# Kernel optimization log

Hardware: AMD Instinct MI355X
Metric: run time of the kernel (lower is better)

## Reference

```python
import jax, jax.numpy as jnp
import numpy as np

N_AG, N_ANCH, C_FEAT, D_ANCH, N_HEAD = 6, 1024, 256, 8, 8


def _ln(x, g, b, eps=1e-5):
    m = x.mean(-1, keepdims=True)
    v = jnp.mean((x - m) ** 2, axis=-1, keepdims=True)
    return (x - m) / jnp.sqrt(v + eps) * g + b


def _forward(i2j_anchor, b_anchor, b_feature, transform_matrix, lidar_range, anchor_embed,
             cls_w1, cls_b1, cls_g1, cls_bb1, cls_w2, cls_b2, cls_g2, cls_bb2, cls_w3, cls_b3,
             bn_g, bn_b, te_w1, te_b1, te_w2, te_b2, ae_w, ae_b, ae_g, ae_bb,
             wq, bq, wk, bk, wv, bv, wo, bo, norm_g, norm_b, K, step):
    N, A, D = b_anchor.shape
    C = b_feature.shape[-1]
    H = N_HEAD
    dh = C // H
    # refinement.cls_layers: [Linear,ReLU,LN] x2 + Linear->1, then sigmoid
    x = _ln(jax.nn.relu(b_feature @ cls_w1 + cls_b1), cls_g1, cls_bb1)
    x = _ln(jax.nn.relu(x @ cls_w2 + cls_b2), cls_g2, cls_bb2)
    roi = jax.nn.sigmoid(x @ cls_w3 + cls_b3)[..., 0]                       # [N,A]
    top_scores, top_idx = jax.lax.top_k(roi, K)                             # [N,K]
    conf_mask = top_scores > 0.7
    neigh_feat = jnp.take_along_axis(b_feature, top_idx[:, :, None], axis=1)  # [N,K,C]
    idx4 = jnp.broadcast_to(top_idx[None, :, :, None], (N, N, K, D))
    i2j = jnp.take_along_axis(i2j_anchor, idx4, axis=2)                     # [N,N,K,D]
    # diagonal removal (static off-diagonal index pattern)
    off = np.nonzero(~np.eye(N, dtype=bool))
    i2j_rm = i2j[off].reshape(N, (N - 1) * K, D)
    tm_rm = transform_matrix[off].reshape(N, N - 1, 4, 4)
    nf_rm = jnp.broadcast_to(neigh_feat[None], (N, N, K, C))[off].reshape(N, (N - 1) * K, C)
    cm_rm = jnp.broadcast_to(conf_mask[None, :, :, None], (N, N, K, 1))[off].reshape(N, (N - 1) * K, 1)
    # transform encoding: BatchNorm1d(12) (training batch stats) + Mlp(12->256->256)
    flat = tm_rm[..., :3, :].reshape(-1, 12)                                # rows 0..2 flattened = stacked 12 entries
    mu = flat.mean(0)
    var = jnp.mean((flat - mu) ** 2, axis=0)
    bn = (flat - mu) / jnp.sqrt(var + 1e-5) * bn_g + bn_b
    te = jax.nn.relu(bn @ te_w1 + te_b1) @ te_w2 + te_b2                    # [N*(N-1),C]
    te = jnp.repeat(te.reshape(N, N - 1, 1, C), K, axis=2).reshape(N, (N - 1) * K, C)
    ae = _ln(jax.nn.relu(i2j_rm @ ae_w + ae_b), ae_g, ae_bb)
    key_pos = ae + te  # computed in the original forward but unused downstream
    # oriented bbox -> axis-aligned corners
    s = jnp.abs(b_anchor[..., 6])
    c = jnp.abs(b_anchor[..., 7])
    dims = jnp.exp(b_anchor[..., 3:6])
    half = jnp.stack([0.5 * (dims[..., 0] * c + dims[..., 1] * s),
                      0.5 * (dims[..., 0] * s + dims[..., 1] * c),
                      0.5 * dims[..., 2]], axis=-1)
    minp = b_anchor[..., :3] - half                                         # [N,A,3]
    maxp = b_anchor[..., :3] + half
    # ego <- neighbor cross attention (residual, query_pos added to query)
    ego = jnp.broadcast_to(b_feature[0:1], (N - 1, A, C))
    neigh = b_feature[1:]
    qpos = jnp.broadcast_to(anchor_embed[0:1], (N - 1, A, C))
    q = ((ego + qpos) @ wq + bq).reshape(N - 1, A, H, dh)
    k = (neigh @ wk + bk).reshape(N - 1, A, H, dh)
    v = (neigh @ wv + bv).reshape(N - 1, A, H, dh)
    scores = jnp.einsum('bqhd,bkhd->bhqk', q, k) / jnp.sqrt(jnp.asarray(dh, q.dtype))
    attn = jax.nn.softmax(scores, axis=-1)
    o = jnp.einsum('bhqk,bkhd->bqhd', attn, v).reshape(N - 1, A, C) @ wo + bo
    res = jnp.sum(ego + o, axis=0, keepdims=True)                           # [1,A,C]
    _ = _ln(res, norm_g, norm_b)  # self.norm(res): computed then overwritten in original
    # confidence-masked neighbor features, bbox-containment aggregation
    nf_rm = nf_rm * cm_rm.astype(nf_rm.dtype)
    pts = i2j_rm[..., :3]                                                   # [N,M,3], M=(N-1)*K
    inside = jnp.all((pts[:, None] >= minp[:, :, None]) & (pts[:, None] <= maxp[:, :, None]), axis=-1)  # [N,A,M]
    cnt = inside.sum(-1)
    agg = jnp.einsum('nam,nmc->nac', inside.astype(nf_rm.dtype), nf_rm) / jnp.maximum(cnt, 1).astype(nf_rm.dtype)[..., None]
    out_feat = res + agg                                                    # [1,A,C] + [N,A,C] -> [N,A,C]
    return b_anchor, out_feat


def setup_inputs():
    N, A, C, D = N_AG, N_ANCH, C_FEAT, D_ANCH
    ks = jax.random.split(jax.random.key(0), 16)
    def nrm(i, shp, s=1.0):
        return s * jax.random.normal(ks[i], shp, dtype=jnp.float32)
    z = lambda *shp: jnp.zeros(shp, jnp.float32)
    o = lambda *shp: jnp.ones(shp, jnp.float32)
    return {
        'i2j_anchor': nrm(0, (N, N, A, D)), 'b_anchor': nrm(1, (N, A, D)),
        'b_feature': nrm(2, (N, A, C)), 'transform_matrix': nrm(3, (N, N, 4, 4)),
        'lidar_range': z(6), 'anchor_embed': nrm(4, (N, A, C)),
        'cls_w1': nrm(5, (C, C), 0.05), 'cls_b1': z(C), 'cls_g1': o(C), 'cls_bb1': z(C),
        'cls_w2': nrm(6, (C, C), 0.05), 'cls_b2': z(C), 'cls_g2': o(C), 'cls_bb2': z(C),
        'cls_w3': nrm(7, (C, 1), 0.05), 'cls_b3': z(1),
        'bn_g': o(12), 'bn_b': z(12),
        'te_w1': nrm(8, (12, C), 0.05), 'te_b1': z(C), 'te_w2': nrm(9, (C, C), 0.05), 'te_b2': z(C),
        'ae_w': nrm(10, (D, C), 0.05), 'ae_b': z(C), 'ae_g': o(C), 'ae_bb': z(C),
        'wq': nrm(11, (C, C), 0.05), 'bq': z(C), 'wk': nrm(12, (C, C), 0.05), 'bk': z(C),
        'wv': nrm(13, (C, C), 0.05), 'bv': z(C), 'wo': nrm(14, (C, C), 0.05), 'bo': z(C),
        'norm_g': o(C), 'norm_b': z(C),
        'K': 256, 'step': 1,
    }


def reference(i2j_anchor, b_anchor, b_feature, transform_matrix, lidar_range, anchor_embed,
              cls_w1, cls_b1, cls_g1, cls_bb1, cls_w2, cls_b2, cls_g2, cls_bb2, cls_w3, cls_b3,
              bn_g, bn_b, te_w1, te_b1, te_w2, te_b2, ae_w, ae_b, ae_g, ae_bb,
              wq, bq, wk, bk, wv, bv, wo, bo, norm_g, norm_b, K, step):
    return _forward(i2j_anchor, b_anchor, b_feature, transform_matrix, lidar_range, anchor_embed,
                    cls_w1, cls_b1, cls_g1, cls_bb1, cls_w2, cls_b2, cls_g2, cls_bb2, cls_w3, cls_b3,
                    bn_g, bn_b, te_w1, te_b1, te_w2, te_b2, ae_w, ae_b, ae_g, ae_bb,
                    wq, bq, wk, bk, wv, bv, wo, bo, norm_g, norm_b, K, step)
```

## Files before the change

kernel.cpp:

```cpp
#include <hip/hip_runtime.h>


#define N_AG   6
#define N_ANCH 1024
#define C_FEAT 256
#define D_ANCH 8
#define KTOP   256
#define NM     1280
#define NR     40960
#define ZROW   393216
#define AC     262144

__device__ __forceinline__ float waveSum(float v) {
  #pragma unroll
  for (int off = 32; off; off >>= 1) v += __shfl_down(v, off);
  return v;
}

__global__ __launch_bounds__(256) void cls_kernel(
    const float* __restrict__ bf,
    const float* __restrict__ w1, const float* __restrict__ b1,
    const float* __restrict__ g1, const float* __restrict__ bb1,
    const float* __restrict__ w2, const float* __restrict__ b2,
    const float* __restrict__ g2, const float* __restrict__ bb2,
    const float* __restrict__ w3, const float* __restrict__ b3,
    float* __restrict__ roi)
{
  __shared__ float xin[8][256];
  __shared__ float xout[8][256];
  __shared__ float stats[8][2];
  const int t = threadIdx.x;
  const int wid = t >> 6, lane = t & 63;
  const int r0 = blockIdx.x * 8;

  for (int r = 0; r < 8; ++r) xin[r][t] = bf[(r0 + r) * 256 + t];

  const float G1 = g1[t], B1 = bb1[t], G2 = g2[t], B2 = bb2[t];
  float acc[8];

  #pragma unroll
  for (int r = 0; r < 8; ++r) acc[r] = b1[t];
  __syncthreads();
  for (int kk = 0; kk < 256; kk += 4) {
    const float wa = w1[(kk+0)*256+t], wb = w1[(kk+1)*256+t];
    const float wc = w1[(kk+2)*256+t], wd = w1[(kk+3)*256+t];
    #pragma unroll
    for (int r = 0; r < 8; ++r) {
      const float4 xv = *(const float4*)&xin[r][kk];
      acc[r] = fmaf(xv.x, wa, fmaf(xv.y, wb, fmaf(xv.z, wc, fmaf(xv.w, wd, acc[r]))));
    }
  }
  #pragma unroll
  for (int r = 0; r < 8; ++r) xout[r][t] = fmaxf(acc[r], 0.f);
  __syncthreads();
  for (int r = wid; r < 8; r += 4) {
    float s = xout[r][lane] + xout[r][lane+64] + xout[r][lane+128] + xout[r][lane+192];
    s = waveSum(s);
    if (lane == 0) stats[r][0] = s * (1.f/256.f);
  }
  __syncthreads();
  for (int r = wid; r < 8; r += 4) {
    const float m = stats[r][0];
    const float d0 = xout[r][lane]-m, d1 = xout[r][lane+64]-m;
    const float d2 = xout[r][lane+128]-m, d3 = xout[r][lane+192]-m;
    const float s = waveSum(d0*d0 + d1*d1 + d2*d2 + d3*d3);
    if (lane == 0) stats[r][1] = 1.f / sqrtf(s * (1.f/256.f) + 1e-5f);
  }
  __syncthreads();
  #pragma unroll
  for (int r = 0; r < 8; ++r)
    xin[r][t] = (xout[r][t] - stats[r][0]) * stats[r][1] * G1 + B1;
  __syncthreads();

  #pragma unroll
  for (int r = 0; r < 8; ++r) acc[r] = b2[t];
  for (int kk = 0; kk < 256; kk += 4) {
    const float wa = w2[(kk+0)*256+t], wb = w2[(kk+1)*256+t];
    const float wc = w2[(kk+2)*256+t], wd = w2[(kk+3)*256+t];
    #pragma unroll
    for (int r = 0; r < 8; ++r) {
      const float4 xv = *(const float4*)&xin[r][kk];
      acc[r] = fmaf(xv.x, wa, fmaf(xv.y, wb, fmaf(xv.z, wc, fmaf(xv.w, wd, acc[r]))));
    }
  }
  __syncthreads();
  #pragma unroll
  for (int r = 0; r < 8; ++r) xout[r][t] = fmaxf(acc[r], 0.f);
  __syncthreads();
  for (int r = wid; r < 8; r += 4) {
    float s = xout[r][lane] + xout[r][lane+64] + xout[r][lane+128] + xout[r][lane+192];
    s = waveSum(s);
    if (lane == 0) stats[r][0] = s * (1.f/256.f);
  }
  __syncthreads();
  for (int r = wid; r < 8; r += 4) {
    const float m = stats[r][0];
    const float d0 = xout[r][lane]-m, d1 = xout[r][lane+64]-m;
    const float d2 = xout[r][lane+128]-m, d3 = xout[r][lane+192]-m;
    const float s = waveSum(d0*d0 + d1*d1 + d2*d2 + d3*d3);
    if (lane == 0) stats[r][1] = 1.f / sqrtf(s * (1.f/256.f) + 1e-5f);
  }
  __syncthreads();
  const float w3t = w3[t], b30 = b3[0];
  #pragma unroll
  for (int r = 0; r < 8; ++r) {
    const float xn = (xout[r][t] - stats[r][0]) * stats[r][1] * G2 + B2;
    xin[r][t] = xn * w3t;
  }
  __syncthreads();
  for (int r = wid; r < 8; r += 4) {
    float s = xin[r][lane] + xin[r][lane+64] + xin[r][lane+128] + xin[r][lane+192];
    s = waveSum(s);
    if (lane == 0) roi[r0 + r] = 1.f / (1.f + expf(-(s + b30)));
  }
}

__global__ __launch_bounds__(512) void topk_kernel(
    const float* __restrict__ roi, int* __restrict__ top_idx, float* __restrict__ conf)
{
  __shared__ unsigned long long keys[1024];
  const int t = threadIdx.x;
  const int ag = blockIdx.x;
  for (int i = t; i < 1024; i += 512) {
    const unsigned int bits = __float_as_uint(roi[ag * 1024 + i]);
    keys[i] = ((unsigned long long)bits << 10) | (unsigned long long)(1023 - i);
  }
  __syncthreads();
  for (int k = 2; k <= 1024; k <<= 1) {
    for (int j = k >> 1; j > 0; j >>= 1) {
      const int i = ((t & ~(j - 1)) << 1) | (t & (j - 1));
      const int p = i | j;
      const unsigned long long a = keys[i], b = keys[p];
      const bool up = ((i & k) == 0);
      if ((a < b) == up) { keys[i] = b; keys[p] = a; }
      __syncthreads();
    }
  }
  if (t < 256) {
    const unsigned long long key = keys[t];
    const int idx = 1023 - (int)(key & 1023ull);
    const float sc = __uint_as_float((unsigned int)(key >> 10));
    top_idx[ag * 256 + t] = idx;
    conf[ag * 256 + t] = (sc > 0.7f) ? 1.0f : 0.0f;
  }
}

__global__ __launch_bounds__(256) void gather_prep_kernel(
    const float* __restrict__ bf, const int* __restrict__ top_idx,
    const float* __restrict__ conf, const float* __restrict__ ba,
    const float* __restrict__ i2j,
    float* __restrict__ mfeat, float* __restrict__ out,
    float* __restrict__ minmax, float* __restrict__ pts)
{
  const int t = threadIdx.x;
  const int blk = blockIdx.x;
  if (blk < 1536) {
    const int j = blk >> 8, idx = top_idx[blk];
    const float c = conf[blk];
    mfeat[blk * 256 + t] = bf[(j * 1024 + idx) * 256 + t] * c;
    return;
  }
  if (blk == 1536) { mfeat[ZROW + t] = 0.f; return; }
  const int id = (blk - 1537) * 256 + t;
  if (id < 49152) {
    out[id] = ba[id];
  } else if (id < 49152 + 6144) {
    const int i = id - 49152;
    const float* p = ba + i * 8;
    const float cx = p[0], cy = p[1], cz = p[2];
    const float d0 = expf(p[3]), d1 = expf(p[4]), d2 = expf(p[5]);
    const float s = fabsf(p[6]), c = fabsf(p[7]);
    const float hx = 0.5f * (d0 * c + d1 * s);
    const float hy = 0.5f * (d0 * s + d1 * c);
    const float hz = 0.5f * d2;
    float* mm = minmax + i * 6;
    mm[0] = cx - hx; mm[1] = cy - hy; mm[2] = cz - hz;
    mm[3] = cx + hx; mm[4] = cy + hy; mm[5] = cz + hz;
  } else if (id < 49152 + 6144 + 7680) {
    const int i = id - 55296;
    const int n = i / NM, jk = i % NM;
    const int jj = jk >> 8, k = jk & 255;
    const int j = jj + (jj >= n ? 1 : 0);
    const int idx = top_idx[j * 256 + k];
    const float* src = i2j + (((long)(n * 6 + j)) * 1024 + idx) * 8;
    float* dst = pts + n * 3840;
    dst[jk]        = src[0];
    dst[1280 + jk] = src[1];
    dst[2560 + jk] = src[2];
  }
}

__global__ __launch_bounds__(256) void qkv_kernel(
    const float* __restrict__ bf, const float* __restrict__ ae,
    const float* __restrict__ wq, const float* __restrict__ bq,
    const float* __restrict__ wk, const float* __restrict__ bk,
    const float* __restrict__ wv, const float* __restrict__ bv,
    float* __restrict__ qb, float* __restrict__ kb, float* __restrict__ vb)
{
  __shared__ float xin[8][256];
  const int t = threadIdx.x;
  const int blk = blockIdx.x;
  const float* in; const float* add = nullptr;
  const float* w; const float* bias; float* outp; long r0;
  if (blk < 128)      { in = bf;      add = ae; w = wq; bias = bq; outp = qb; r0 = (long)blk * 8; }
  else if (blk < 768) { in = bf + AC;           w = wk; bias = bk; outp = kb; r0 = (long)(blk - 128) * 8; }
  else                { in = bf + AC;           w = wv; bias = bv; outp = vb; r0 = (long)(blk - 768) * 8; }

  for (int r = 0; r < 8; ++r) {
    float v = in[(r0 + r) * 256 + t];
    if (add) v += add[(r0 + r) * 256 + t];
    xin[r][t] = v;
  }
  __syncthreads();
  float acc[8];
  #pragma unroll
  for (int r = 0; r < 8; ++r) acc[r] = bias[t];
  for (int kk = 0; kk < 256; kk += 4) {
    const float wa = w[(kk+0)*256+t], wb = w[(kk+1)*256+t];
    const float wc = w[(kk+2)*256+t], wd = w[(kk+3)*256+t];
    #pragma unroll
    for (int r = 0; r < 8; ++r) {
      const float4 xv = *(const float4*)&xin[r][kk];
      acc[r] = fmaf(xv.x, wa, fmaf(xv.y, wb, fmaf(xv.z, wc, fmaf(xv.w, wd, acc[r]))));
    }
  }
  for (int r = 0; r < 8; ++r) outp[(r0 + r) * 256 + t] = acc[r];
}

template<int SPLITS>
__global__ __launch_bounds__(256) void attn_kernel(
    const float* __restrict__ q, const float* __restrict__ kb,
    const float* __restrict__ vb, float* __restrict__ po,
    float* __restrict__ pml, float* __restrict__ ob)
{
  __shared__ float ks[128][32];
  __shared__ float vs[128][32];
  const int t = threadIdx.x;
  const int h = blockIdx.y;
  const int b = blockIdx.z / SPLITS;
  const int split = blockIdx.z % SPLITS;
  const int qid = blockIdx.x * 256 + t;
  const int hh = h * 32;
  const float SCALE = 0.17677669529663687f;
  float qv[32];
  #pragma unroll
  for (int d0 = 0; d0 < 32; d0 += 4) {
    const float4 v = *(const float4*)&q[qid * 256 + hh + d0];
    qv[d0] = v.x * SCALE; qv[d0+1] = v.y * SCALE;
    qv[d0+2] = v.z * SCALE; qv[d0+3] = v.w * SCALE;
  }
  float m = -1e30f, l = 0.f;
  float o[32];
  #pragma unroll
  for (int d = 0; d < 32; ++d) o[d] = 0.f;
  const float* kbase = kb + (long)b * 1024 * 256;
  const float* vbase = vb + (long)b * 1024 * 256;
  const int KEYS = 1024 / SPLITS;
  const int k0 = split * KEYS;
  for (int c0 = k0; c0 < k0 + KEYS; c0 += 128) {
    __syncthreads();
    for (int i = t; i < 1024; i += 256) {
      const int kk = i >> 3, d = (i & 7) << 2;
      *(float4*)&ks[kk][d] = *(const float4*)&kbase[(c0 + kk) * 256 + hh + d];
    }
    for (int i = t; i < 1024; i += 256) {
      const int kk = i >> 3, d = (i & 7) << 2;
      *(float4*)&vs[kk][d] = *(const float4*)&vbase[(c0 + kk) * 256 + hh + d];
    }
    __syncthreads();
    #pragma unroll 1
    for (int kk0 = 0; kk0 < 128; kk0 += 16) {
      float s[16];
      #pragma unroll
      for (int u = 0; u < 16; ++u) {
        const float* krow = &ks[kk0 + u][0];
        float a = 0.f;
        #pragma unroll
        for (int d = 0; d < 32; ++d) a = fmaf(qv[d], krow[d], a);
        s[u] = a;
      }
      float cmax = s[0];
      #pragma unroll
      for (int u = 1; u < 16; ++u) cmax = fmaxf(cmax, s[u]);
      if (cmax > m) {
        const float sc = __expf(m - cmax);
        l *= sc;
        #pragma unroll
        for (int d = 0; d < 32; ++d) o[d] *= sc;
        m = cmax;
      }
      #pragma unroll
      for (int u = 0; u < 16; ++u) {
        const float p = __expf(s[u] - m);
        l += p;
        const float* vrow = &vs[kk0 + u][0];
        #pragma unroll
        for (int d = 0; d < 32; ++d) o[d] = fmaf(p, vrow[d], o[d]);
      }
    }
  }
  if (SPLITS == 1) {
    const float inv = 1.f / l;
    float* dst = ob + ((long)b * 1024 + qid) * 256 + hh;
    #pragma unroll
    for (int d = 0; d < 32; d += 4) {
      float4 v;
      v.x = o[d] * inv; v.y = o[d+1] * inv; v.z = o[d+2] * inv; v.w = o[d+3] * inv;
      *(float4*)&dst[d] = v;
    }
  } else {
    const int R = (b * 8 + h) * 1024 + qid;
    float* pd = po + ((long)split * NR + R) * 32;
    #pragma unroll
    for (int d = 0; d < 32; d += 4) {
      float4 v; v.x = o[d]; v.y = o[d+1]; v.z = o[d+2]; v.w = o[d+3];
      *(float4*)&pd[d] = v;
    }
    float* pm = pml + ((long)split * NR + R) * 2;
    pm[0] = m; pm[1] = l;
  }
}

template<int SPLITS>
__global__ __launch_bounds__(256) void attn_combine_kernel(
    const float* __restrict__ po, const float* __restrict__ pml,
    float* __restrict__ ob)
{
  const int id = blockIdx.x * 256 + threadIdx.x;
  const int R = id >> 5, d = id & 31;
  float M = -1e30f;
  #pragma unroll
  for (int s = 0; s < SPLITS; ++s)
    M = fmaxf(M, pml[((long)s * NR + R) * 2]);
  float L = 0.f, O = 0.f;
  #pragma unroll
  for (int s = 0; s < SPLITS; ++s) {
    const float w = __expf(pml[((long)s * NR + R) * 2] - M);
    L += pml[((long)s * NR + R) * 2 + 1] * w;
    O += po[((long)s * NR + R) * 32 + d] * w;
  }
  const int b = R >> 13, h = (R >> 10) & 7, qq = R & 1023;
  ob[((long)(b * 1024 + qq)) * 256 + h * 32 + d] = O / L;
}

__global__ __launch_bounds__(256) void res_kernel(
    const float* __restrict__ obuf, const float* __restrict__ bf,
    const float* __restrict__ wo, const float* __restrict__ bo,
    float* __restrict__ res)
{
  __shared__ float xin[4][256];
  const int t = threadIdx.x;
  const int r0 = blockIdx.x * 4;
  for (int r = 0; r < 4; ++r) {
    const long a = r0 + r;
    float v = 0.f;
    #pragma unroll
    for (int b = 0; b < 5; ++b) v += obuf[(b * 1024 + a) * 256 + t];
    xin[r][t] = v;
  }
  __syncthreads();
  float acc[4];
  #pragma unroll
  for (int r = 0; r < 4; ++r) acc[r] = 0.f;
  for (int kk = 0; kk < 256; kk += 4) {
    const float wa = wo[(kk+0)*256+t], wb = wo[(kk+1)*256+t];
    const float wc = wo[(kk+2)*256+t], wd = wo[(kk+3)*256+t];
    #pragma unroll
    for (int r = 0; r < 4; ++r) {
      const float4 xv = *(const float4*)&xin[r][kk];
      acc[r] = fmaf(xv.x, wa, fmaf(xv.y, wb, fmaf(xv.z, wc, fmaf(xv.w, wd, acc[r]))));
    }
  }
  const float bot = 5.f * bo[t];
  for (int r = 0; r < 4; ++r)
    res[(r0 + r) * 256 + t] = acc[r] + bot + 5.f * bf[(r0 + r) * 256 + t];
}

__global__ __launch_bounds__(256) void agg_kernel(
    const float* __restrict__ pts, const float* __restrict__ minmax,
    const float* __restrict__ conf, const float* __restrict__ mfeat,
    const float* __restrict__ res, float* __restrict__ outf)
{
  __shared__ int list[NM];
  __shared__ int wcnt[4];
  __shared__ int wicnt[4];
  const int t = threadIdx.x, w = t >> 6, lane = t & 63;
  const int n = blockIdx.x >> 10;
  const int a = blockIdx.x & 1023;

  const float* mm = minmax + (n * 1024 + a) * 6;
  const float mnx = mm[0], mny = mm[1], mnz = mm[2];
  const float mxx = mm[3], mxy = mm[4], mxz = mm[5];

  const float* P = pts + n * 3840;
  int localBase = 0, insideCnt = 0;
  #pragma unroll
  for (int s = 0; s < 5; ++s) {
    const int mpt = w * 320 + s * 64 + lane;
    const float x = P[mpt], y = P[1280 + mpt], z = P[2560 + mpt];
    const bool in = (x >= mnx) & (x <= mxx) & (y >= mny) & (y <= mxy) &
                    (z >= mnz) & (z <= mxz);
    const int jj = mpt >> 8;
    const int j = jj + (jj >= n ? 1 : 0);
    const int row = (j << 8) | (mpt & 255);
    const bool keep = in && (conf[row] > 0.f);
    const unsigned long long kmask = __ballot(keep);
    if (keep)
      list[w * 320 + localBase + __popcll(kmask & ((1ull << lane) - 1ull))] = row << 8;
    localBase += __popcll(kmask);
    insideCnt += __popcll(__ballot(in));
  }
  const int nwp = (localBase + 3) & ~3;
  if (lane < nwp - localBase) list[w * 320 + localBase + lane] = ZROW;
  if (lane == 0) { wcnt[w] = nwp; wicnt[w] = insideCnt; }
  __syncthreads();

  const int cnt = wicnt[0] + wicnt[1] + wicnt[2] + wicnt[3];
  float a0 = 0.f, a1 = 0.f, a2 = 0.f, a3 = 0.f;
  const float* mf = mfeat + t;
  #pragma unroll 1
  for (int ww = 0; ww < 4; ++ww) {
    const int base = ww * 320, nw = wcnt[ww];
    #pragma unroll 1
    for (int l = 0; l < nw; l += 4) {
      const int o0 = list[base + l],     o1 = list[base + l + 1];
      const int o2 = list[base + l + 2], o3 = list[base + l + 3];
      a0 += mf[o0]; a1 += mf[o1];
      a2 += mf[o2]; a3 += mf[o3];
    }
  }
  const float acc = (a0 + a1) + (a2 + a3);
  outf[((long)(n * 1024 + a)) * 256 + t] =
      res[a * 256 + t] + acc / (float)(cnt > 0 ? cnt : 1);
}

extern "C" void kernel_launch(void* const* d_in, const int* in_sizes, int n_in,
                              void* d_out, int out_size, void* d_ws, size_t ws_size,
                              hipStream_t stream)
{
  (void)in_sizes; (void)n_in; (void)out_size;
  const float* i2j_anchor  = (const float*)d_in[0];
  const float* b_anchor    = (const float*)d_in[1];
  const float* b_feature   = (const float*)d_in[2];
  const float* anchor_embed= (const float*)d_in[5];
  const float* cls_w1 = (const float*)d_in[6];
  const float* cls_b1 = (const float*)d_in[7];
  const float* cls_g1 = (const float*)d_in[8];
  const float* cls_bb1= (const float*)d_in[9];
  const float* cls_w2 = (const float*)d_in[10];
  const float* cls_b2 = (const float*)d_in[11];
  const float* cls_g2 = (const float*)d_in[12];
  const float* cls_bb2= (const float*)d_in[13];
  const float* cls_w3 = (const float*)d_in[14];
  const float* cls_b3 = (const float*)d_in[15];
  const float* wq = (const float*)d_in[26];
  const float* bq = (const float*)d_in[27];
  const float* wk = (const float*)d_in[28];
  const float* bk = (const float*)d_in[29];
  const float* wv = (const float*)d_in[30];
  const float* bv = (const float*)d_in[31];
  const float* wo = (const float*)d_in[32];
  const float* bo = (const float*)d_in[33];
  float* out = (float*)d_out;

  float* ws = (float*)d_ws;
  float* roi    = ws;
  int*   tidx   = (int*)(ws + 6144);
  float* conf   = ws + 7680;
  float* mfeat  = ws + 9216;
  float* qbuf   = ws + 402688;
  float* kbuf   = ws + 664832;
  float* vbuf   = ws + 1975552;
  float* obuf   = ws + 3286272;
  float* resbuf = ws + 4596992;
  float* minmax = ws + 4859136;
  float* pts    = ws + 4896000;
  float* pml8 = ws + 4919040;
  float* po8  = ws + 5574400;
  float* pml4 = ws + 4919040;
  float* po4  = ws + 5246720;
  const size_t need8  = (size_t)16060160 * sizeof(float);
  const size_t need4  = (size_t)10489600 * sizeof(float);

  cls_kernel<<<768, 256, 0, stream>>>(b_feature, cls_w1, cls_b1, cls_g1, cls_bb1,
                                      cls_w2, cls_b2, cls_g2, cls_bb2,
                                      cls_w3, cls_b3, roi);
  topk_kernel<<<6, 512, 0, stream>>>(roi, tidx, conf);
  gather_prep_kernel<<<1783, 256, 0, stream>>>(b_feature, tidx, conf, b_anchor,
                                               i2j_anchor, mfeat, out, minmax, pts);
  qkv_kernel<<<1408, 256, 0, stream>>>(b_feature, anchor_embed,
                                       wq, bq, wk, bk, wv, bv, qbuf, kbuf, vbuf);
  if (ws_size >= need8) {
    attn_kernel<8><<<dim3(4, 8, 40), 256, 0, stream>>>(qbuf, kbuf, vbuf, po8, pml8, nullptr);
    attn_combine_kernel<8><<<NR * 32 / 256, 256, 0, stream>>>(po8, pml8, obuf);
  } else if (ws_size >= need4) {
    attn_kernel<4><<<dim3(4, 8, 20), 256, 0, stream>>>(qbuf, kbuf, vbuf, po4, pml4, nullptr);
    attn_combine_kernel<4><<<NR * 32 / 256, 256, 0, stream>>>(po4, pml4, obuf);
  } else {
    attn_kernel<1><<<dim3(4, 8, 5), 256, 0, stream>>>(qbuf, kbuf, vbuf, nullptr, nullptr, obuf);
  }
  res_kernel<<<256, 256, 0, stream>>>(obuf, b_feature, wo, bo, resbuf);
  agg_kernel<<<6144, 256, 0, stream>>>(pts, minmax, conf, mfeat, resbuf, out + 49152);
}
```

Baseline: 394.4 us.

## Rewrite attention with bf16 MFMA flash kernel and head-major bf16 QKV layout

The QKV projection now writes Q (pre-scaled), K and a transposed V as bf16 in per-head layouts. The scalar fp32 split-K attention and its combine pass are replaced by a single-wave flash-attention kernel that uses 16x16x32 bf16 MFMA for both QK^T and PV, with an online softmax and register prefetch of the next K/V tile. This removes the fp32 FMA-bound attention and the partial-result round trip through memory, at the cost of bf16 precision in the scores and probabilities.

```diff
diff --git a/kernel.cpp b/kernel.cpp
--- a/kernel.cpp
+++ b/kernel.cpp
@@ -7,14 +7,21 @@
 #define D_ANCH 8
 #define KTOP   256
 #define NM     1280
-#define NR     40960
 #define ZROW   393216
 #define AC     262144
 
+using short8 = __attribute__((ext_vector_type(8))) short;
+using f32x4  = __attribute__((ext_vector_type(4))) float;
+
 __device__ __forceinline__ float waveSum(float v) {
   #pragma unroll
   for (int off = 32; off; off >>= 1) v += __shfl_down(v, off);
   return v;
+}
+
+__device__ __forceinline__ unsigned short f2bf(float x) {
+  const unsigned int b = __float_as_uint(x);
+  return (unsigned short)((b + 0x7FFFu + ((b >> 16) & 1u)) >> 16);
 }
 
 __global__ __launch_bounds__(256) void cls_kernel(
@@ -195,16 +202,18 @@
     const float* __restrict__ wq, const float* __restrict__ bq,
     const float* __restrict__ wk, const float* __restrict__ bk,
     const float* __restrict__ wv, const float* __restrict__ bv,
-    float* __restrict__ qb, float* __restrict__ kb, float* __restrict__ vb)
+    unsigned short* __restrict__ qb16, unsigned short* __restrict__ kb16,
+    unsigned short* __restrict__ vt16)
 {
   __shared__ float xin[8][256];
   const int t = threadIdx.x;
   const int blk = blockIdx.x;
   const float* in; const float* add = nullptr;
-  const float* w; const float* bias; float* outp; long r0;
-  if (blk < 128)      { in = bf;      add = ae; w = wq; bias = bq; outp = qb; r0 = (long)blk * 8; }
-  else if (blk < 768) { in = bf + AC;           w = wk; bias = bk; outp = kb; r0 = (long)(blk - 128) * 8; }
-  else                { in = bf + AC;           w = wv; bias = bv; outp = vb; r0 = (long)(blk - 768) * 8; }
+  const float* w; const float* bias; long r0;
+  int mode;
+  if (blk < 128)      { in = bf;      add = ae; w = wq; bias = bq; r0 = (long)blk * 8;        mode = 0; }
+  else if (blk < 768) { in = bf + AC;           w = wk; bias = bk; r0 = (long)(blk - 128) * 8; mode = 1; }
+  else                { in = bf + AC;           w = wv; bias = bv; r0 = (long)(blk - 768) * 8; mode = 2; }
 
   for (int r = 0; r < 8; ++r) {
     float v = in[(r0 + r) * 256 + t];
@@ -224,123 +233,104 @@
       acc[r] = fmaf(xv.x, wa, fmaf(xv.y, wb, fmaf(xv.z, wc, fmaf(xv.w, wd, acc[r]))));
     }
   }
-  for (int r = 0; r < 8; ++r) outp[(r0 + r) * 256 + t] = acc[r];
-}
-
-template<int SPLITS>
-__global__ __launch_bounds__(256) void attn_kernel(
-    const float* __restrict__ q, const float* __restrict__ kb,
-    const float* __restrict__ vb, float* __restrict__ po,
-    float* __restrict__ pml, float* __restrict__ ob)
-{
-  __shared__ float ks[128][32];
-  __shared__ float vs[128][32];
-  const int t = threadIdx.x;
-  const int h = blockIdx.y;
-  const int b = blockIdx.z / SPLITS;
-  const int split = blockIdx.z % SPLITS;
-  const int qid = blockIdx.x * 256 + t;
-  const int hh = h * 32;
-  const float SCALE = 0.17677669529663687f;
-  float qv[32];
-  #pragma unroll
-  for (int d0 = 0; d0 < 32; d0 += 4) {
-    const float4 v = *(const float4*)&q[qid * 256 + hh + d0];
-    qv[d0] = v.x * SCALE; qv[d0+1] = v.y * SCALE;
-    qv[d0+2] = v.z * SCALE; qv[d0+3] = v.w * SCALE;
-  }
-  float m = -1e30f, l = 0.f;
-  float o[32];
-  #pragma unroll
-  for (int d = 0; d < 32; ++d) o[d] = 0.f;
-  const float* kbase = kb + (long)b * 1024 * 256;
-  const float* vbase = vb + (long)b * 1024 * 256;
-  const int KEYS = 1024 / SPLITS;
-  const int k0 = split * KEYS;
-  for (int c0 = k0; c0 < k0 + KEYS; c0 += 128) {
+  const int h = t >> 5, d = t & 31;
+  if (mode == 0) {
+    const float SCALE = 0.17677669529663687f;
+    #pragma unroll
+    for (int r = 0; r < 8; ++r)
+      qb16[(long)h * 32768 + (r0 + r) * 32 + d] = f2bf(acc[r] * SCALE);
+  } else if (mode == 1) {
+    #pragma unroll
+    for (int r = 0; r < 8; ++r) {
+      const long row = r0 + r;
+      const int b = (int)(row >> 10), kkk = (int)(row & 1023);
+      kb16[((long)(b * 8 + h)) * 32768 + kkk * 32 + d] = f2bf(acc[r]);
+    }
+  } else {
+    const int b = (int)(r0 >> 10), kk0 = (int)(r0 & 1023);
+    short8 v8;
+    #pragma unroll
+    for (int r = 0; r < 8; ++r) v8[r] = (short)f2bf(acc[r]);
+    *(short8*)&vt16[((long)(b * 8 + h)) * 32768 + (long)d * 1024 + kk0] = v8;
+  }
+}
+
+__global__ __launch_bounds__(64) void attn_kernel(
+    const unsigned short* __restrict__ qb,
+    const unsigned short* __restrict__ kb,
+    const unsigned short* __restrict__ vt,
+    float* __restrict__ ob)
+{
+  __shared__ unsigned short pls[2][16][32];
+  const int l = threadIdx.x;
+  const int qt = blockIdx.x, h = blockIdx.y, b = blockIdx.z;
+  const int bh = b * 8 + h;
+  const int r16 = l & 15, g = l >> 4;
+
+  const short8 qf = *(const short8*)(qb + (long)h * 32768 + (qt * 16 + r16) * 32 + 8 * g);
+  const unsigned short* kbase = kb + (long)bh * 32768;
+  const unsigned short* vbase = vt + (long)bh * 32768;
+
+  f32x4 oc0 = {0.f, 0.f, 0.f, 0.f};
+  f32x4 oc1 = {0.f, 0.f, 0.f, 0.f};
+  float m[4]    = {-1e30f, -1e30f, -1e30f, -1e30f};
+  float lsum[4] = {0.f, 0.f, 0.f, 0.f};
+
+  short8 kf0 = *(const short8*)(kbase + (r16) * 32 + 8 * g);
+  short8 kf1 = *(const short8*)(kbase + (16 + r16) * 32 + 8 * g);
+  short8 vf0 = *(const short8*)(vbase + (long)r16 * 1024 + 8 * g);
+  short8 vf1 = *(const short8*)(vbase + (long)(16 + r16) * 1024 + 8 * g);
+
+  #pragma unroll 1
+  for (int K0 = 0; K0 < 1024; K0 += 32) {
+    const int Kn = (K0 + 32 < 1024) ? K0 + 32 : 0;
+    const short8 nk0 = *(const short8*)(kbase + (Kn + r16) * 32 + 8 * g);
+    const short8 nk1 = *(const short8*)(kbase + (Kn + 16 + r16) * 32 + 8 * g);
+    const short8 nv0 = *(const short8*)(vbase + (long)r16 * 1024 + Kn + 8 * g);
+    const short8 nv1 = *(const short8*)(vbase + (long)(16 + r16) * 1024 + Kn + 8 * g);
+
+    const f32x4 z = {0.f, 0.f, 0.f, 0.f};
+    f32x4 s0 = __builtin_amdgcn_mfma_f32_16x16x32_bf16(qf, kf0, z, 0, 0, 0);
+    f32x4 s1 = __builtin_amdgcn_mfma_f32_16x16x32_bf16(qf, kf1, z, 0, 0, 0);
+
+    const int buf = (K0 >> 5) & 1;
+    #pragma unroll
+    for (int r = 0; r < 4; ++r) {
+      float mx = fmaxf(s0[r], s1[r]);
+      mx = fmaxf(mx, __shfl_xor(mx, 1));
+      mx = fmaxf(mx, __shfl_xor(mx, 2));
+      mx = fmaxf(mx, __shfl_xor(mx, 4));
+      mx = fmaxf(mx, __shfl_xor(mx, 8));
+      const float nm = fmaxf(m[r], mx);
+      const float sc = __expf(m[r] - nm);
+      m[r] = nm;
+      const float p0 = __expf(s0[r] - nm);
+      const float p1 = __expf(s1[r] - nm);
+      float rs = p0 + p1;
+      rs += __shfl_xor(rs, 1);
+      rs += __shfl_xor(rs, 2);
+      rs += __shfl_xor(rs, 4);
+      rs += __shfl_xor(rs, 8);
+      lsum[r] = lsum[r] * sc + rs;
+      oc0[r] *= sc; oc1[r] *= sc;
+      pls[buf][4 * g + r][r16]      = f2bf(p0);
+      pls[buf][4 * g + r][16 + r16] = f2bf(p1);
+    }
     __syncthreads();
-    for (int i = t; i < 1024; i += 256) {
-      const int kk = i >> 3, d = (i & 7) << 2;
-      *(float4*)&ks[kk][d] = *(const float4*)&kbase[(c0 + kk) * 256 + hh + d];
-    }
-    for (int i = t; i < 1024; i += 256) {
-      const int kk = i >> 3, d = (i & 7) << 2;
-      *(float4*)&vs[kk][d] = *(const float4*)&vbase[(c0 + kk) * 256 + hh + d];
-    }
-    __syncthreads();
-    #pragma unroll 1
-    for (int kk0 = 0; kk0 < 128; kk0 += 16) {
-      float s[16];
-      #pragma unroll
-      for (int u = 0; u < 16; ++u) {
-        const float* krow = &ks[kk0 + u][0];
-        float a = 0.f;
-        #pragma unroll
-        for (int d = 0; d < 32; ++d) a = fmaf(qv[d], krow[d], a);
-        s[u] = a;
-      }
-      float cmax = s[0];
-      #pragma unroll
-      for (int u = 1; u < 16; ++u) cmax = fmaxf(cmax, s[u]);
-      if (cmax > m) {
-        const float sc = __expf(m - cmax);
-        l *= sc;
-        #pragma unroll
-        for (int d = 0; d < 32; ++d) o[d] *= sc;
-        m = cmax;
-      }
-      #pragma unroll
-      for (int u = 0; u < 16; ++u) {
-        const float p = __expf(s[u] - m);
-        l += p;
-        const float* vrow = &vs[kk0 + u][0];
-        #pragma unroll
-        for (int d = 0; d < 32; ++d) o[d] = fmaf(p, vrow[d], o[d]);
-      }
-    }
-  }
-  if (SPLITS == 1) {
-    const float inv = 1.f / l;
-    float* dst = ob + ((long)b * 1024 + qid) * 256 + hh;
-    #pragma unroll
-    for (int d = 0; d < 32; d += 4) {
-      float4 v;
-      v.x = o[d] * inv; v.y = o[d+1] * inv; v.z = o[d+2] * inv; v.w = o[d+3] * inv;
-      *(float4*)&dst[d] = v;
-    }
-  } else {
-    const int R = (b * 8 + h) * 1024 + qid;
-    float* pd = po + ((long)split * NR + R) * 32;
-    #pragma unroll
-    for (int d = 0; d < 32; d += 4) {
-      float4 v; v.x = o[d]; v.y = o[d+1]; v.z = o[d+2]; v.w = o[d+3];
-      *(float4*)&pd[d] = v;
-    }
-    float* pm = pml + ((long)split * NR + R) * 2;
-    pm[0] = m; pm[1] = l;
-  }
-}
-
-template<int SPLITS>
-__global__ __launch_bounds__(256) void attn_combine_kernel(
-    const float* __restrict__ po, const float* __restrict__ pml,
-    float* __restrict__ ob)
-{
-  const int id = blockIdx.x * 256 + threadIdx.x;
-  const int R = id >> 5, d = id & 31;
-  float M = -1e30f;
-  #pragma unroll
-  for (int s = 0; s < SPLITS; ++s)
-    M = fmaxf(M, pml[((long)s * NR + R) * 2]);
-  float L = 0.f, O = 0.f;
-  #pragma unroll
-  for (int s = 0; s < SPLITS; ++s) {
-    const float w = __expf(pml[((long)s * NR + R) * 2] - M);
-    L += pml[((long)s * NR + R) * 2 + 1] * w;
-    O += po[((long)s * NR + R) * 32 + d] * w;
-  }
-  const int b = R >> 13, h = (R >> 10) & 7, qq = R & 1023;
-  ob[((long)(b * 1024 + qq)) * 256 + h * 32 + d] = O / L;
+    const short8 pf = *(const short8*)&pls[buf][r16][8 * g];
+    oc0 = __builtin_amdgcn_mfma_f32_16x16x32_bf16(pf, vf0, oc0, 0, 0, 0);
+    oc1 = __builtin_amdgcn_mfma_f32_16x16x32_bf16(pf, vf1, oc1, 0, 0, 0);
+    kf0 = nk0; kf1 = nk1; vf0 = nv0; vf1 = nv1;
+  }
+
+  float* dst = ob + ((long)(b * 1024 + qt * 16)) * 256 + h * 32;
+  #pragma unroll
+  for (int r = 0; r < 4; ++r) {
+    const float inv = 1.f / lsum[r];
+    const int row = 4 * g + r;
+    dst[row * 256 + r16]      = oc0[r] * inv;
+    dst[row * 256 + 16 + r16] = oc1[r] * inv;
+  }
 }
 
 __global__ __launch_bounds__(256) void res_kernel(
@@ -438,7 +428,7 @@
                               void* d_out, int out_size, void* d_ws, size_t ws_size,
                               hipStream_t stream)
 {
-  (void)in_sizes; (void)n_in; (void)out_size;
+  (void)in_sizes; (void)n_in; (void)out_size; (void)ws_size;
   const float* i2j_anchor  = (const float*)d_in[0];
   const float* b_anchor    = (const float*)d_in[1];
   const float* b_feature   = (const float*)d_in[2];
@@ -468,19 +458,13 @@
   int*   tidx   = (int*)(ws + 6144);
   float* conf   = ws + 7680;
   float* mfeat  = ws + 9216;
-  float* qbuf   = ws + 402688;
-  float* kbuf   = ws + 664832;
-  float* vbuf   = ws + 1975552;
-  float* obuf   = ws + 3286272;
-  float* resbuf = ws + 4596992;
-  float* minmax = ws + 4859136;
-  float* pts    = ws + 4896000;
-  float* pml8 = ws + 4919040;
-  float* po8  = ws + 5574400;
-  float* pml4 = ws + 4919040;
-  float* po4  = ws + 5246720;
-  const size_t need8  = (size_t)16060160 * sizeof(float);
-  const size_t need4  = (size_t)10489600 * sizeof(float);
+  float* obuf   = ws + 402688;
+  float* resbuf = ws + 1713408;
+  float* minmax = ws + 1975552;
+  float* pts    = ws + 2012416;
+  unsigned short* qb16 = (unsigned short*)(ws + 2035456);
+  unsigned short* kb16 = (unsigned short*)(ws + 2166528);
+  unsigned short* vt16 = (unsigned short*)(ws + 2821888);
 
   cls_kernel<<<768, 256, 0, stream>>>(b_feature, cls_w1, cls_b1, cls_g1, cls_bb1,
                                       cls_w2, cls_b2, cls_g2, cls_bb2,
@@ -489,16 +473,8 @@
   gather_prep_kernel<<<1783, 256, 0, stream>>>(b_feature, tidx, conf, b_anchor,
                                                i2j_anchor, mfeat, out, minmax, pts);
   qkv_kernel<<<1408, 256, 0, stream>>>(b_feature, anchor_embed,
-                                       wq, bq, wk, bk, wv, bv, qbuf, kbuf, vbuf);
-  if (ws_size >= need8) {
-    attn_kernel<8><<<dim3(4, 8, 40), 256, 0, stream>>>(qbuf, kbuf, vbuf, po8, pml8, nullptr);
-    attn_combine_kernel<8><<<NR * 32 / 256, 256, 0, stream>>>(po8, pml8, obuf);
-  } else if (ws_size >= need4) {
-    attn_kernel<4><<<dim3(4, 8, 20), 256, 0, stream>>>(qbuf, kbuf, vbuf, po4, pml4, nullptr);
-    attn_combine_kernel<4><<<NR * 32 / 256, 256, 0, stream>>>(po4, pml4, obuf);
-  } else {
-    attn_kernel<1><<<dim3(4, 8, 5), 256, 0, stream>>>(qbuf, kbuf, vbuf, nullptr, nullptr, obuf);
-  }
+                                       wq, bq, wk, bk, wv, bv, qb16, kb16, vt16);
+  attn_kernel<<<dim3(64, 8, 5), 64, 0, stream>>>(qb16, kb16, vt16, obuf);
   res_kernel<<<256, 256, 0, stream>>>(obuf, b_feature, wo, bo, resbuf);
   agg_kernel<<<6144, 256, 0, stream>>>(pts, minmax, conf, mfeat, resbuf, out + 49152);
 }
```

After: 336.4 us. 14.7% less time.
